# Kernel tuning notes

Measured on AMD Instinct MI355X. Metric: run time of the kernel, lower is better.

## Reference

```python
import jax, jax.numpy as jnp
import numpy as np

D_MODEL = 512
OUT_MODEL = 512
NUM_HEADS = 8
D_K = OUT_MODEL // NUM_HEADS


def setup_inputs() -> dict:
    key = jax.random.key(0)
    ks = jax.random.split(key, 11)
    B, S = 4, 2048
    inp = {
        "Q": jax.random.normal(ks[0], (B, S, D_MODEL), dtype=jnp.float32),
        "K": jax.random.normal(ks[1], (B, S, D_MODEL), dtype=jnp.float32),
        "V": jax.random.normal(ks[2], (B, S, D_MODEL), dtype=jnp.float32),
    }
    sc = 1.0 / np.sqrt(D_MODEL)
    inp["Wq"] = jax.random.normal(ks[3], (D_MODEL, OUT_MODEL), dtype=jnp.float32) * sc
    inp["bq"] = jnp.zeros((OUT_MODEL,), dtype=jnp.float32)
    inp["Wk"] = jax.random.normal(ks[4], (D_MODEL, OUT_MODEL), dtype=jnp.float32) * sc
    inp["bk"] = jnp.zeros((OUT_MODEL,), dtype=jnp.float32)
    inp["Wv"] = jax.random.normal(ks[5], (D_MODEL, OUT_MODEL), dtype=jnp.float32) * sc
    inp["bv"] = jnp.zeros((OUT_MODEL,), dtype=jnp.float32)
    inp["Wo"] = jax.random.normal(ks[6], (OUT_MODEL, OUT_MODEL), dtype=jnp.float32) * sc
    inp["bo"] = jnp.zeros((OUT_MODEL,), dtype=jnp.float32)
    return inp


def _split_heads(x):
    B, S, _ = x.shape
    return x.reshape(B, S, NUM_HEADS, D_K).transpose(0, 2, 1, 3)  # [B,H,S,Dk]


def reference(Q, K, V, Wq, bq, Wk, bk, Wv, bv, Wo, bo):
    q = _split_heads(Q @ Wq + bq)
    k = _split_heads(K @ Wk + bk)
    v = _split_heads(V @ Wv + bv)
    scores = jnp.einsum("bhsd,bhtd->bhst", q, k) / jnp.sqrt(jnp.float32(D_K))
    probs = jax.nn.softmax(scores, axis=-1)
    attn = jnp.einsum("bhst,bhtd->bhsd", probs, v)  # [B,H,S,Dk]
    B, H, S, Dk = attn.shape
    merged = attn.transpose(0, 2, 1, 3).reshape(B, S, OUT_MODEL)
    return merged @ Wo + bo
```

## Files before the change

### kernel.cpp

```cpp
#include <hip/hip_runtime.h>
#include <hip/hip_bf16.h>
#include <cstdint>


using short8 = __attribute__((ext_vector_type(8))) short;
using f32x4  = __attribute__((ext_vector_type(4))) float;
using f32x16 = __attribute__((ext_vector_type(16))) float;

#define DEVINL __device__ __forceinline__

constexpr int BB  = 4;
constexpr int SS  = 2048;
constexpr int DM  = 512;
constexpr int NH  = 8;
constexpr int DKH = 64;
constexpr float C2 = 0.18033688011112042f;

DEVINL unsigned short f2bf(float f) {
    __hip_bfloat16 h = __float2bfloat16(f);
    return *reinterpret_cast<unsigned short*>(&h);
}

DEVINL f32x4 mfma16(short8 a, short8 b, f32x4 c) {
    return __builtin_amdgcn_mfma_f32_16x16x32_bf16(a, b, c, 0, 0, 0);
}
DEVINL f32x16 mfma32(short8 a, short8 b, f32x16 c) {
    return __builtin_amdgcn_mfma_f32_32x32x16_bf16(a, b, c, 0, 0, 0);
}

DEVINL void gl16(const void* g, void* l) {
    __builtin_amdgcn_global_load_lds(
        (const __attribute__((address_space(1))) unsigned int*)g,
        (__attribute__((address_space(3))) unsigned int*)l, 16, 0, 0);
}
DEVINL void vmcnt0() { asm volatile("s_waitcnt vmcnt(0)" ::: "memory"); }

DEVINL unsigned cvtpk(float a, float b) {
    unsigned r;
    asm("v_cvt_pk_bf16_f32 %0, %1, %2" : "=v"(r) : "v"(a), "v"(b));
    return r;
}

__global__ __launch_bounds__(256)
void prep_w(const float* __restrict__ Wq, const float* __restrict__ Wk,
            const float* __restrict__ Wv, const float* __restrict__ Wo,
            unsigned short* __restrict__ wt)
{
    const int z = blockIdx.z;
    const float* W = (z == 0) ? Wq : (z == 1) ? Wk : (z == 2) ? Wv : Wo;
    unsigned short* Wtz = wt + (size_t)z * DM * DM;

    __shared__ unsigned short T[64][72];
    const int t = threadIdx.x;
    const int k0 = blockIdx.x * 64, n0 = blockIdx.y * 64;
    const int r = t >> 2, cs = t & 3;

    #pragma unroll
    for (int q = 0; q < 4; ++q) {
        float4 v = *reinterpret_cast<const float4*>(
            &W[(size_t)(k0 + r) * DM + n0 + cs * 16 + q * 4]);
        union { unsigned short u[4]; unsigned long long ll; } pk;
        pk.u[0] = f2bf(v.x); pk.u[1] = f2bf(v.y);
        pk.u[2] = f2bf(v.z); pk.u[3] = f2bf(v.w);
        *reinterpret_cast<unsigned long long*>(&T[r][cs * 16 + q * 4]) = pk.ll;
    }
    __syncthreads();
    union { unsigned short u[8]; short8 v; } p0, p1;
    #pragma unroll
    for (int e = 0; e < 8; ++e) p0.u[e] = T[cs * 16 + e][r];
    #pragma unroll
    for (int e = 0; e < 8; ++e) p1.u[e] = T[cs * 16 + 8 + e][r];
    *reinterpret_cast<short8*>(&Wtz[(size_t)(n0 + r) * DM + k0 + cs * 16]) = p0.v;
    *reinterpret_cast<short8*>(&Wtz[(size_t)(n0 + r) * DM + k0 + cs * 16 + 8]) = p1.v;
}

__global__ __launch_bounds__(256, 4)
void qkv_proj_kernel(const float* __restrict__ Qin, const float* __restrict__ Kin,
                     const float* __restrict__ Vin,
                     const unsigned short* __restrict__ wt,
                     const float* __restrict__ bq, const float* __restrict__ bk,
                     const float* __restrict__ bv,
                     unsigned short* __restrict__ qb, unsigned short* __restrict__ kb2,
                     unsigned short* __restrict__ vt2)
{
    const int z = blockIdx.z;
    const float* A           = (z == 0) ? Qin : (z == 1) ? Kin : Vin;
    const unsigned short* Wt = wt + (size_t)z * DM * DM;
    const float* bias        = (z == 0) ? bq : (z == 1) ? bk : bv;

    __shared__ unsigned short SMEM[16384];

    const int tid = threadIdx.x, lane = tid & 63, w = tid >> 6;
    const int wm = w >> 1, wn = w & 1;
    const int row16 = lane & 15, kg = lane >> 4;
    const int m0tok = blockIdx.x * 128, n0ch = blockIdx.y * 128;

    const int ar = tid >> 1, ah = tid & 1;

    float4 apf[4];
    auto load_A = [&](int kt) {
        const float* Ap = &A[(size_t)(m0tok + ar) * DM + kt * 32 + ah * 16];
        #pragma unroll
        for (int q = 0; q < 4; ++q)
            apf[q] = *reinterpret_cast<const float4*>(Ap + q * 4);
    };
    auto write_A = [&](int buf) {
        #pragma unroll
        for (int s = 0; s < 2; ++s) {
            union { unsigned short u[8]; short8 v; } pk;
            float4 a = apf[2 * s], b = apf[2 * s + 1];
            pk.u[0] = f2bf(a.x); pk.u[1] = f2bf(a.y);
            pk.u[2] = f2bf(a.z); pk.u[3] = f2bf(a.w);
            pk.u[4] = f2bf(b.x); pk.u[5] = f2bf(b.y);
            pk.u[6] = f2bf(b.z); pk.u[7] = f2bf(b.w);
            int phys = (ah * 2 + s) ^ (ar & 3);
            *reinterpret_cast<short8*>(&SMEM[buf * 4096 + ar * 32 + phys * 8]) = pk.v;
        }
    };
    auto issue_B = [&](int kt, int buf) {
        #pragma unroll
        for (int i = 0; i < 2; ++i) {
            int chunk = tid + i * 256;
            int n = chunk >> 2, c = chunk & 3;
            const unsigned short* src =
                &Wt[(size_t)(n0ch + n) * DM + kt * 32 + ((c ^ (n & 3)) * 8)];
            gl16(src, (char*)SMEM + 16384 + (size_t)buf * 8192 +
                      (size_t)(w * 64 + i * 256) * 16);
        }
    };

    f32x4 acc[4][4] = {};
    const int aoff = ((z == 2) ? wn : wm) * 64;
    const int boff = ((z == 2) ? wm : wn) * 64;

    load_A(0); issue_B(0, 0);
    vmcnt0();
    write_A(0);
    __syncthreads();

    for (int t = 0; t < 16; ++t) {
        const int cur = t & 1, nxt = cur ^ 1;
        if (t + 1 < 16) { issue_B(t + 1, nxt); load_A(t + 1); }

        short8 af[4], bfr[4];
        #pragma unroll
        for (int i = 0; i < 4; ++i) {
            int ra = aoff + i * 16 + row16;
            int rb = boff + i * 16 + row16;
            af[i]  = *reinterpret_cast<const short8*>(
                &SMEM[cur * 4096 + ra * 32 + ((kg ^ (ra & 3)) * 8)]);
            bfr[i] = *reinterpret_cast<const short8*>(
                &SMEM[8192 + cur * 4096 + rb * 32 + ((kg ^ (rb & 3)) * 8)]);
        }
        __builtin_amdgcn_s_setprio(1);
        #pragma unroll
        for (int mf = 0; mf < 4; ++mf)
            #pragma unroll
            for (int nf = 0; nf < 4; ++nf)
                acc[mf][nf] = (z == 2)
                    ? mfma16(bfr[mf], af[nf], acc[mf][nf])
                    : mfma16(af[mf], bfr[nf], acc[mf][nf]);
        __builtin_amdgcn_s_setprio(0);

        vmcnt0();
        if (t + 1 < 16) write_A(nxt);
        __syncthreads();
    }

    if (z == 0) {
        #pragma unroll
        for (int nf = 0; nf < 4; ++nf) {
            int ch = n0ch + wn * 64 + nf * 16 + row16;
            float bval = bias[ch];
            int h = ch >> 6, dk = ch & 63;
            #pragma unroll
            for (int mf = 0; mf < 4; ++mf)
                #pragma unroll
                for (int j = 0; j < 4; ++j) {
                    int tok = m0tok + wm * 64 + mf * 16 + kg * 4 + j;
                    int b = tok >> 11, s = tok & 2047;
                    qb[(((size_t)b * NH + h) * SS + s) * DKH + dk] =
                        f2bf((acc[mf][nf][j] + bval) * C2);
                }
        }
    } else {
        __syncthreads();
        if (z == 1) {
            #pragma unroll
            for (int nf = 0; nf < 4; ++nf) {
                int dk = nf * 16 + row16;
                float bval = bias[n0ch + wn * 64 + dk];
                #pragma unroll
                for (int mf = 0; mf < 4; ++mf)
                    #pragma unroll
                    for (int j = 0; j < 4; ++j) {
                        int s6 = mf * 16 + kg * 4 + j;
                        SMEM[w * 4096 + (dk >> 3) * 512 + s6 * 8 + (dk & 7)] =
                            f2bf(acc[mf][nf][j] + bval);
                    }
            }
        } else {
            const int tile = wn * 2 + wm;
            #pragma unroll
            for (int mf = 0; mf < 4; ++mf)
                #pragma unroll
                for (int j = 0; j < 4; ++j) {
                    int dk6 = mf * 16 + kg * 4 + j;
                    float bval = bias[n0ch + wm * 64 + dk6];
                    #pragma unroll
                    for (int nf = 0; nf < 4; ++nf) {
                        int s6 = nf * 16 + row16;
                        SMEM[tile * 4096 + (s6 >> 3) * 512 + dk6 * 8 + (s6 & 7)] =
                            f2bf(acc[mf][nf][j] + bval);
                    }
                }
        }
        __syncthreads();
        const int sblk = m0tok + (w >> 1) * 64;
        const int hg   = (n0ch >> 6) + (w & 1);
        const int b    = sblk >> 11, s_in_b = sblk & 2047;
        unsigned short* dst =
            ((z == 1) ? kb2 : vt2) +
            ((size_t)(b * NH + hg)) * (SS * DKH) + (size_t)(s_in_b >> 6) * 4096;
        #pragma unroll
        for (int i = 0; i < 8; ++i)
            *reinterpret_cast<short8*>(&dst[i * 512 + lane * 8]) =
                *reinterpret_cast<const short8*>(&SMEM[w * 4096 + i * 512 + lane * 8]);
    }
}

__global__ __launch_bounds__(512, 4)
void attn_kernel(const unsigned short* __restrict__ qb,
                 const unsigned short* __restrict__ kb2,
                 const unsigned short* __restrict__ vt2,
                 unsigned short* __restrict__ am)
{
    __shared__ unsigned short Ks[2][2][4096];
    __shared__ unsigned short Vs[2][2][4096];

    const int tid = threadIdx.x, lane = tid & 63, w = tid >> 6;
    const int wq = w & 3, hf = w >> 2;
    const int l31 = lane & 31, hi = lane >> 5;
    const int bh = blockIdx.y, b = bh >> 3, h = bh & 7;
    const int q0 = blockIdx.x * 128;
    const size_t base = (size_t)bh * (SS * DKH);
    const int tile0 = hf * 16;

    auto stage_KV = [&](int tl) {
        const int tt = tile0 + tl, buf = tl & 1;
        const unsigned short* ksrc = kb2 + base + (size_t)tt * 4096;
        const unsigned short* vsrc = vt2 + base + (size_t)tt * 4096;
        #pragma unroll
        for (int i = 0; i < 2; ++i) {
            int cb = i * 256 + wq * 64;
            gl16(ksrc + (size_t)(cb + lane) * 8,
                 (char*)Ks[hf][buf] + (size_t)cb * 16);
            gl16(vsrc + (size_t)(cb + lane) * 8,
                 (char*)Vs[hf][buf] + (size_t)cb * 16);
        }
    };

    short8 qf[4];
    const int qrow = q0 + wq * 32 + l31;
    #pragma unroll
    for (int ks = 0; ks < 4; ++ks)
        qf[ks] = *reinterpret_cast<const short8*>(
            &qb[base + (size_t)qrow * DKH + (ks * 2 + hi) * 8]);
    vmcnt0();

    stage_KV(0);
    __syncthreads();

    f32x16 o[2] = {};
    float lsum = 0.f;
    unsigned pk[2][4][2];

    auto do_QK = [&](int buf, f32x16 (&sfr)[2]) {
        #pragma unroll
        for (int ks = 0; ks < 4; ++ks) {
            int c = ks * 2 + hi;
            #pragma unroll
            for (int mkv = 0; mkv < 2; ++mkv) {
                short8 kf = *reinterpret_cast<const short8*>(
                    &Ks[hf][buf][(c * 64 + mkv * 32 + l31) * 8]);
                sfr[mkv] = mfma32(kf, qf[ks], sfr[mkv]);
            }
        }
    };
    auto do_softmax = [&](const f32x16 (&sfr)[2]) {
        #pragma unroll
        for (int mkv = 0; mkv < 2; ++mkv)
            #pragma unroll
            for (int bq = 0; bq < 4; ++bq) {
                float p0 = __builtin_amdgcn_exp2f(sfr[mkv][bq * 4 + 0]);
                float p1 = __builtin_amdgcn_exp2f(sfr[mkv][bq * 4 + 1]);
                float p2 = __builtin_amdgcn_exp2f(sfr[mkv][bq * 4 + 2]);
                float p3 = __builtin_amdgcn_exp2f(sfr[mkv][bq * 4 + 3]);
                lsum += (p0 + p1) + (p2 + p3);
                pk[mkv][bq][0] = cvtpk(p0, p1);
                pk[mkv][bq][1] = cvtpk(p2, p3);
            }
    };
    auto do_PV = [&](int buf) {
        #pragma unroll
        for (int ks2 = 0; ks2 < 4; ++ks2) {
            const int mkv = ks2 >> 1, b0 = (ks2 & 1) * 2, b1 = b0 + 1;
            unsigned x0 = pk[mkv][b0][0], y0 = pk[mkv][b1][0];
            unsigned x1 = pk[mkv][b0][1], y1 = pk[mkv][b1][1];
            asm volatile("v_permlane32_swap_b32 %0, %1" : "+v"(x0), "+v"(y0));
            asm volatile("v_permlane32_swap_b32 %0, %1" : "+v"(x1), "+v"(y1));
            union { unsigned u[4]; short8 s; } pa;
            pa.u[0] = x0; pa.u[1] = x1; pa.u[2] = y0; pa.u[3] = y1;
            int c = ks2 * 2 + hi;
            #pragma unroll
            for (int ndk = 0; ndk < 2; ++ndk) {
                short8 vf = *reinterpret_cast<const short8*>(
                    &Vs[hf][buf][(c * 64 + ndk * 32 + l31) * 8]);
                o[ndk] = mfma32(pa.s, vf, o[ndk]);
            }
        }
    };

    for (int tl = 0; tl < 16; ++tl) {
        if (tl < 15) stage_KV(tl + 1);
        const int buf = tl & 1;

        f32x16 sfr[2] = {};
        __builtin_amdgcn_s_setprio(1);
        do_QK(buf, sfr);
        __builtin_amdgcn_s_setprio(0);
        do_softmax(sfr);
        __builtin_amdgcn_s_setprio(1);
        do_PV(buf);
        __builtin_amdgcn_s_setprio(0);

        if (tl < 15) __syncthreads();
    }

    __syncthreads();
    float* comb  = reinterpret_cast<float*>(&Ks[0][0][0]);
    float* lcomb = reinterpret_cast<float*>(&Vs[0][0][0]);
    if (hf == 1) {
        #pragma unroll
        for (int ndk = 0; ndk < 2; ++ndk)
            #pragma unroll
            for (int r = 0; r < 16; ++r)
                comb[((wq * 2 + ndk) * 16 + r) * 64 + lane] = o[ndk][r];
        lcomb[wq * 64 + lane] = lsum;
    }
    __syncthreads();
    if (hf == 0) {
        lsum += lcomb[wq * 64 + lane];
        float lfull = lsum + __shfl_xor(lsum, 32, 64);
        float linv = 1.0f / lfull;
        #pragma unroll
        for (int ndk = 0; ndk < 2; ++ndk)
            #pragma unroll
            for (int r = 0; r < 16; ++r)
                o[ndk][r] += comb[((wq * 2 + ndk) * 16 + r) * 64 + lane];
        #pragma unroll
        for (int r = 0; r < 16; ++r) {
            int qloc = (r & 3) + 8 * (r >> 2) + 4 * hi;
            float li = __shfl(linv, qloc, 64);
            int sg = q0 + wq * 32 + qloc;
            #pragma unroll
            for (int ndk = 0; ndk < 2; ++ndk) {
                int dk = ndk * 32 + l31;
                am[((size_t)b * SS + sg) * DM + h * DKH + dk] =
                    f2bf(o[ndk][r] * li);
            }
        }
    }
}

__global__ __launch_bounds__(256, 4)
void out_proj_kernel(const unsigned short* __restrict__ am,
                     const unsigned short* __restrict__ Wt,
                     const float* __restrict__ bo,
                     float* __restrict__ out)
{
    __shared__ unsigned short As[2][64 * 32];
    __shared__ unsigned short Bs[2][128 * 32];

    const int tid = threadIdx.x, lane = tid & 63, w = tid >> 6;
    const int wm = w & 1, wn = w >> 1;
    const int row16 = lane & 15, kg = lane >> 4;
    const int m0 = blockIdx.x * 64;
    const int n0 = blockIdx.y * 128;

    auto stage = [&](int kt, int buf) {
        {
            int r = tid >> 2, c = tid & 3;
            gl16(&am[(size_t)(m0 + r) * DM + kt * 32 + ((c ^ (r & 3)) * 8)],
                 (char*)As + (size_t)buf * 4096 + (size_t)(w * 64) * 16);
        }
        #pragma unroll
        for (int i = 0; i < 2; ++i) {
            int cc = tid + i * 256;
            int n = cc >> 2, c = cc & 3;
            gl16(&Wt[(size_t)(n0 + n) * DM + kt * 32 + ((c ^ (n & 3)) * 8)],
                 (char*)Bs + (size_t)buf * 8192 + (size_t)(w * 64 + i * 256) * 16);
        }
    };

    f32x4 acc[2][4] = {};

    stage(0, 0);
    vmcnt0();
    __syncthreads();

    for (int t = 0; t < 16; ++t) {
        const int cur = t & 1, nxt = cur ^ 1;
        if (t + 1 < 16) stage(t + 1, nxt);

        short8 af[2], bfr[4];
        #pragma unroll
        for (int i = 0; i < 2; ++i) {
            int ra = wm * 32 + i * 16 + row16;
            af[i] = *reinterpret_cast<const short8*>(
                &As[cur][ra * 32 + ((kg ^ (ra & 3)) * 8)]);
        }
        #pragma unroll
        for (int i = 0; i < 4; ++i) {
            int rb = wn * 64 + i * 16 + row16;
            bfr[i] = *reinterpret_cast<const short8*>(
                &Bs[cur][rb * 32 + ((kg ^ (rb & 3)) * 8)]);
        }
        __builtin_amdgcn_s_setprio(1);
        #pragma unroll
        for (int mf = 0; mf < 2; ++mf)
            #pragma unroll
            for (int nf = 0; nf < 4; ++nf)
                acc[mf][nf] = mfma16(af[mf], bfr[nf], acc[mf][nf]);
        __builtin_amdgcn_s_setprio(0);

        vmcnt0();
        __syncthreads();
    }

    #pragma unroll
    for (int nf = 0; nf < 4; ++nf) {
        int n = n0 + wn * 64 + nf * 16 + row16;
        float bval = bo[n];
        #pragma unroll
        for (int mf = 0; mf < 2; ++mf)
            #pragma unroll
            for (int j = 0; j < 4; ++j) {
                int mrow = m0 + wm * 32 + mf * 16 + kg * 4 + j;
                out[(size_t)mrow * DM + n] = acc[mf][nf][j] + bval;
            }
    }
}

extern "C" void kernel_launch(void* const* d_in, const int* in_sizes, int n_in,
                              void* d_out, int out_size, void* d_ws, size_t ws_size,
                              hipStream_t stream) {
    const float* Q  = (const float*)d_in[0];
    const float* K  = (const float*)d_in[1];
    const float* V  = (const float*)d_in[2];
    const float* Wq = (const float*)d_in[3];
    const float* bq = (const float*)d_in[4];
    const float* Wk = (const float*)d_in[5];
    const float* bk = (const float*)d_in[6];
    const float* Wv = (const float*)d_in[7];
    const float* bv = (const float*)d_in[8];
    const float* Wo = (const float*)d_in[9];
    const float* bo = (const float*)d_in[10];
    float* out = (float*)d_out;

    const size_t per = (size_t)BB * NH * SS * DKH;
    unsigned short* qb  = (unsigned short*)d_ws;
    unsigned short* kb2 = qb + per;
    unsigned short* vt2 = kb2 + per;
    unsigned short* am  = vt2 + per;
    unsigned short* wt  = am + per;

    prep_w<<<dim3(8, 8, 4), 256, 0, stream>>>(Wq, Wk, Wv, Wo, wt);
    qkv_proj_kernel<<<dim3(64, 4, 3), 256, 0, stream>>>(
        Q, K, V, wt, bq, bk, bv, qb, kb2, vt2);
    attn_kernel<<<dim3(SS / 128, BB * NH), 512, 0, stream>>>(qb, kb2, vt2, am);
    out_proj_kernel<<<dim3(128, 4), 256, 0, stream>>>(
        am, wt + 3 * (size_t)DM * DM, bo, out);
}
```

Before: 87.53 us.

## Single-buffer K/V shared tiles to double attention kernel occupancy

Replaces the double-buffered K/V shared-memory tiles with a single buffer per half, cutting LDS use roughly in half, and raises the launch-bounds minimum blocks per CU from 4 to 8. Prefetching of the next K/V tile is dropped: each tile is loaded after a barrier and then waited on with a second barrier. The intent is to hide load latency through more resident blocks instead of in-block overlap. This risks exposed memory latency, an extra barrier per iteration, and register pressure or spills from the tighter launch bound.

```diff
diff --git a/kernel.cpp b/kernel.cpp
--- a/kernel.cpp
+++ b/kernel.cpp
@@ -229,14 +229,13 @@
     }
 }
 
-__global__ __launch_bounds__(512, 4)
+__global__ __launch_bounds__(512, 8)
 void attn_kernel(const unsigned short* __restrict__ qb,
                  const unsigned short* __restrict__ kb2,
                  const unsigned short* __restrict__ vt2,
                  unsigned short* __restrict__ am)
 {
-    __shared__ unsigned short Ks[2][2][4096];
-    __shared__ unsigned short Vs[2][2][4096];
+    __shared__ unsigned short SMEM[16896];
 
     const int tid = threadIdx.x, lane = tid & 63, w = tid >> 6;
     const int wq = w & 3, hf = w >> 2;
@@ -244,19 +243,19 @@
     const int bh = blockIdx.y, b = bh >> 3, h = bh & 7;
     const int q0 = blockIdx.x * 128;
     const size_t base = (size_t)bh * (SS * DKH);
-    const int tile0 = hf * 16;
+
+    unsigned short* Kb = SMEM + hf * 4096;
+    unsigned short* Vb = SMEM + 8192 + hf * 4096;
 
     auto stage_KV = [&](int tl) {
-        const int tt = tile0 + tl, buf = tl & 1;
+        const int tt = hf * 16 + tl;
         const unsigned short* ksrc = kb2 + base + (size_t)tt * 4096;
         const unsigned short* vsrc = vt2 + base + (size_t)tt * 4096;
         #pragma unroll
         for (int i = 0; i < 2; ++i) {
             int cb = i * 256 + wq * 64;
-            gl16(ksrc + (size_t)(cb + lane) * 8,
-                 (char*)Ks[hf][buf] + (size_t)cb * 16);
-            gl16(vsrc + (size_t)(cb + lane) * 8,
-                 (char*)Vs[hf][buf] + (size_t)cb * 16);
+            gl16(ksrc + (size_t)(cb + lane) * 8, (char*)Kb + (size_t)cb * 16);
+            gl16(vsrc + (size_t)(cb + lane) * 8, (char*)Vb + (size_t)cb * 16);
         }
     };
 
@@ -275,14 +274,14 @@
     float lsum = 0.f;
     unsigned pk[2][4][2];
 
-    auto do_QK = [&](int buf, f32x16 (&sfr)[2]) {
+    auto do_QK = [&](f32x16 (&sfr)[2]) {
         #pragma unroll
         for (int ks = 0; ks < 4; ++ks) {
             int c = ks * 2 + hi;
             #pragma unroll
             for (int mkv = 0; mkv < 2; ++mkv) {
                 short8 kf = *reinterpret_cast<const short8*>(
-                    &Ks[hf][buf][(c * 64 + mkv * 32 + l31) * 8]);
+                    &Kb[(c * 64 + mkv * 32 + l31) * 8]);
                 sfr[mkv] = mfma32(kf, qf[ks], sfr[mkv]);
             }
         }
@@ -301,7 +300,7 @@
                 pk[mkv][bq][1] = cvtpk(p2, p3);
             }
     };
-    auto do_PV = [&](int buf) {
+    auto do_PV = [&]() {
         #pragma unroll
         for (int ks2 = 0; ks2 < 4; ++ks2) {
             const int mkv = ks2 >> 1, b0 = (ks2 & 1) * 2, b1 = b0 + 1;
@@ -315,31 +314,32 @@
             #pragma unroll
             for (int ndk = 0; ndk < 2; ++ndk) {
                 short8 vf = *reinterpret_cast<const short8*>(
-                    &Vs[hf][buf][(c * 64 + ndk * 32 + l31) * 8]);
+                    &Vb[(c * 64 + ndk * 32 + l31) * 8]);
                 o[ndk] = mfma32(pa.s, vf, o[ndk]);
             }
         }
     };
 
     for (int tl = 0; tl < 16; ++tl) {
-        if (tl < 15) stage_KV(tl + 1);
-        const int buf = tl & 1;
-
         f32x16 sfr[2] = {};
         __builtin_amdgcn_s_setprio(1);
-        do_QK(buf, sfr);
+        do_QK(sfr);
         __builtin_amdgcn_s_setprio(0);
         do_softmax(sfr);
         __builtin_amdgcn_s_setprio(1);
-        do_PV(buf);
+        do_PV();
         __builtin_amdgcn_s_setprio(0);
 
-        if (tl < 15) __syncthreads();
-    }
-
-    __syncthreads();
-    float* comb  = reinterpret_cast<float*>(&Ks[0][0][0]);
-    float* lcomb = reinterpret_cast<float*>(&Vs[0][0][0]);
+        if (tl < 15) {
+            __syncthreads();
+            stage_KV(tl + 1);
+            __syncthreads();
+        }
+    }
+
+    __syncthreads();
+    float* comb  = reinterpret_cast<float*>(SMEM);
+    float* lcomb = reinterpret_cast<float*>(SMEM + 16384);
     if (hf == 1) {
         #pragma unroll
         for (int ndk = 0; ndk < 2; ++ndk)
```

New measurement: 209.8 us. 140% more time.
